# Kernel tuning notes

Hardware: AMD Instinct MI355X
Metric: run time of the kernel (lower is better)

## Reference

```python
import jax, jax.numpy as jnp
import numpy as np

B, S, D, H, E, K = 2, 2048, 1024, 4096, 8, 2


def setup_inputs() -> dict:
    key = jax.random.key(0)
    ks = jax.random.split(key, 5)
    x = jax.random.normal(ks[0], (B, S, D), dtype=jnp.float32)
    W = 0.02 * jax.random.normal(ks[1], (H, D), dtype=jnp.float32)
    bias = 0.02 * jax.random.normal(ks[2], (H,), dtype=jnp.float32)
    # alpha initialized near 1 (nn.Parameter(torch.ones(...)) + learned perturbation)
    alpha = 1.0 + 0.02 * jax.random.normal(ks[3], (E, D), dtype=jnp.float32)
    beta = 0.02 * jax.random.normal(ks[4], (E, D), dtype=jnp.float32)
    return {"x": x, "W": W, "bias": bias, "alpha": alpha, "beta": beta}


def reference(x, W, bias, alpha, beta):
    """MoEXLayer eval-mode forward (sparsity-aware routing + expert combine).

    x: [B,S,D], W: [H,D], bias: [H], alpha/beta: [E,D]. Returns [B,S,H].
    """
    E = alpha.shape[0]
    # --- Router: per-virtual-expert Gaussian pre-activation statistics ---
    # reconstructed_weight(alpha, beta) = W * alpha + beta  (column-wise affine)
    W_rec = W[None, :, :] * alpha[:, None, :] + beta[:, None, :]      # [E,H,D]
    mu_w = W_rec.mean(axis=1)                                          # [E,D]
    var_w = W_rec.var(axis=1)                                          # [E,D] (unbiased=False)
    mu_h = jnp.einsum('bsd,ed->bse', x, mu_w) + bias.mean()            # [B,S,E]
    sigma_h = jnp.sqrt(jnp.einsum('bsd,ed->bse', x * x, var_w) + 1e-8) # [B,S,E]
    router_logits = jax.lax.erf(mu_h / (jnp.sqrt(2.0) * sigma_h))      # [B,S,E]

    # --- Top-k routing: softmax over top-k logits, zeros elsewhere ---
    topk_vals, topk_idx = jax.lax.top_k(router_logits, K)              # [B,S,K]
    topk_w = jax.nn.softmax(topk_vals, axis=-1)                        # [B,S,K]
    router_weights = (jax.nn.one_hot(topk_idx, E, dtype=x.dtype)
                      * topk_w[..., None]).sum(axis=-2)                # [B,S,E]

    # --- Expert compute + combine (dispatch passes alpha only => beta=0) ---
    W_disp = W[None, :, :] * alpha[:, None, :]                         # [E,H,D]
    pre = jnp.einsum('bsd,ehd->bseh', x, W_disp) + bias                # [B,S,E,H]
    expert_out = jax.nn.relu(pre)
    out = jnp.einsum('bseh,bse->bsh', expert_out, router_weights)      # [B,S,H]
    return out
```

## Files before the change

### kernel.cpp

```cpp
#include <hip/hip_runtime.h>
#include <hip/hip_bf16.h>
#include <math.h>

#define DD 1024
#define HH 4096
#define EE 8
#define MTOK 4096
#define MROWS 8192

typedef __attribute__((ext_vector_type(8))) short bf16x8;
typedef __attribute__((ext_vector_type(4))) float f32x4;

__device__ __forceinline__ unsigned short f2bf(float x){
  __hip_bfloat16 h = __float2bfloat16(x);
  return *reinterpret_cast<unsigned short*>(&h);
}

__device__ __forceinline__ void gload16(const void* g, void* l){
  __builtin_amdgcn_global_load_lds((__attribute__((address_space(1))) void*)g,
                                   (__attribute__((address_space(3))) void*)l,
                                   16, 0, 0);
}

__global__ void cvt_w_kernel(const float4* __restrict__ W4, ushort4* __restrict__ Wb4){
  int i = blockIdx.x * 256 + threadIdx.x;
  float4 v = W4[i];
  ushort4 o;
  o.x = f2bf(v.x); o.y = f2bf(v.y); o.z = f2bf(v.z); o.w = f2bf(v.w);
  Wb4[i] = o;
}

__global__ void colstats_part_kernel(const float4* __restrict__ W4,
                                     float* __restrict__ pmean, float* __restrict__ pm2){
  int rc = blockIdx.x;
  int tid = threadIdx.x;
  double s0=0,s1=0,s2_=0,s3=0, q0=0,q1=0,q2=0,q3=0;
  for (int h = rc * 32; h < rc * 32 + 32; ++h){
    float4 w = W4[(size_t)h * 256 + tid];
    s0 += w.x; q0 += (double)w.x * w.x;
    s1 += w.y; q1 += (double)w.y * w.y;
    s2_ += w.z; q2 += (double)w.z * w.z;
    s3 += w.w; q3 += (double)w.w * w.w;
  }
  int d0 = rc * DD + tid * 4;
  pmean[d0]   = (float)s0;  pm2[d0]   = (float)q0;
  pmean[d0+1] = (float)s1;  pm2[d0+1] = (float)q1;
  pmean[d0+2] = (float)s2_; pm2[d0+2] = (float)q2;
  pmean[d0+3] = (float)s3;  pm2[d0+3] = (float)q3;
}

__global__ void colstats_final_kernel(const float* __restrict__ pmean,
                                      const float* __restrict__ pm2,
                                      double* __restrict__ cmean, double* __restrict__ cvar){
  int d = blockIdx.x * 256 + threadIdx.x;
  double s = 0.0, s2 = 0.0;
  for (int c = 0; c < 128; ++c){ s += (double)pmean[c * DD + d]; s2 += (double)pm2[c * DD + d]; }
  double m = s / (double)HH;
  cmean[d] = m;
  cvar[d]  = s2 / (double)HH - m * m;
}

__global__ void biasmean_kernel(const float* __restrict__ bias, double* __restrict__ bmean){
  __shared__ double red[256];
  double s = 0.0;
  for (int h = threadIdx.x; h < HH; h += 256) s += (double)bias[h];
  red[threadIdx.x] = s;
  __syncthreads();
  for (int k = 128; k > 0; k >>= 1){
    if (threadIdx.x < k) red[threadIdx.x] += red[threadIdx.x + k];
    __syncthreads();
  }
  if (threadIdx.x == 0) *bmean = red[0] / (double)HH;
}

__global__ void muvw_kernel(const float* __restrict__ alpha, const float* __restrict__ beta,
                            const double* __restrict__ cmean, const double* __restrict__ cvar,
                            float* __restrict__ muw, float* __restrict__ vw){
  int i = blockIdx.x * 256 + threadIdx.x;
  int d = i & (DD - 1);
  double a = (double)alpha[i];
  muw[i] = (float)(a * cmean[d] + (double)beta[i]);
  vw[i]  = (float)(a * a * cvar[d]);
}

__global__ __launch_bounds__(256) void router_kernel(const float4* __restrict__ x4,
                                                     const float4* __restrict__ alpha4,
                                                     const float4* __restrict__ muw4,
                                                     const float4* __restrict__ vw4,
                                                     const double* __restrict__ bmeanp,
                                                     unsigned short* __restrict__ Xs,
                                                     float2* __restrict__ wpair){
  int wv = threadIdx.x >> 6, lane = threadIdx.x & 63;
  int t = blockIdx.x * 4 + wv;
  const float4* xt = x4 + (size_t)t * 256;

  float4 xv[4];
  double mu[EE], s2[EE];
  #pragma unroll
  for (int e = 0; e < EE; ++e){ mu[e] = 0.0; s2[e] = 0.0; }

  #pragma unroll
  for (int r = 0; r < 4; ++r){
    int c = lane + 64 * r;
    float4 xf = xt[c];
    xv[r] = xf;
    float x2x = xf.x * xf.x, x2y = xf.y * xf.y, x2z = xf.z * xf.z, x2w = xf.w * xf.w;
    #pragma unroll
    for (int e = 0; e < EE; ++e){
      float4 m4 = muw4[e * 256 + c];
      float4 v4 = vw4[e * 256 + c];
      mu[e] += (double)xf.x * m4.x + (double)xf.y * m4.y
             + (double)xf.z * m4.z + (double)xf.w * m4.w;
      s2[e] += (double)x2x * v4.x + (double)x2y * v4.y
             + (double)x2z * v4.z + (double)x2w * v4.w;
    }
  }

  #pragma unroll
  for (int off = 32; off > 0; off >>= 1){
    #pragma unroll
    for (int e = 0; e < EE; ++e){
      mu[e] += __shfl_xor(mu[e], off);
      s2[e] += __shfl_xor(s2[e], off);
    }
  }

  double bm = *bmeanp;
  double z[EE];
  #pragma unroll
  for (int e = 0; e < EE; ++e){
    double m = mu[e] + bm;
    double v = s2[e] + 1e-8;
    z[e] = m / sqrt(2.0 * v);
  }
  int e1 = 0;
  #pragma unroll
  for (int e = 1; e < EE; ++e) if (z[e] > z[e1]) e1 = e;
  int e2 = -1;
  #pragma unroll
  for (int e = 0; e < EE; ++e){
    if (e == e1) continue;
    if (e2 < 0 || z[e] > z[e2]) e2 = e;
  }
  double lg1 = erf(z[e1]), lg2 = erf(z[e2]);
  double ex = exp(lg2 - lg1);
  float w1 = (float)(1.0 / (1.0 + ex));
  float w2 = (float)(ex / (1.0 + ex));
  if (lane == 0) wpair[t] = make_float2(w1, w2);

  const float4* a1 = alpha4 + (size_t)e1 * 256;
  const float4* a2 = alpha4 + (size_t)e2 * 256;
  ushort4* X1 = (ushort4*)(Xs + (size_t)(2 * t) * DD);
  ushort4* X2 = (ushort4*)(Xs + (size_t)(2 * t + 1) * DD);
  #pragma unroll
  for (int r = 0; r < 4; ++r){
    int c = lane + 64 * r;
    float4 xf = xv[r];
    float4 av = a1[c];
    X1[c] = make_ushort4(f2bf(xf.x * av.x), f2bf(xf.y * av.y),
                         f2bf(xf.z * av.z), f2bf(xf.w * av.w));
    av = a2[c];
    X2[c] = make_ushort4(f2bf(xf.x * av.x), f2bf(xf.y * av.y),
                         f2bf(xf.z * av.z), f2bf(xf.w * av.w));
  }
}

#define BM 128
#define BN 128
#define BK 32

__global__ __launch_bounds__(256) void gemm_kernel(const unsigned short* __restrict__ Xs,
                                                   const unsigned short* __restrict__ Wb,
                                                   const float* __restrict__ bias,
                                                   const float2* __restrict__ wpair,
                                                   float* __restrict__ out){
  __shared__ __align__(16) unsigned short As[BM * BK];
  __shared__ __align__(16) unsigned short Bs[BN * BK];

  int tid = threadIdx.x;
  int lane = tid & 63;
  int wv = tid >> 6;
  int wr = wv >> 1, wc = wv & 1;

  int bid = blockIdx.x;
  int swz = ((bid & 7) << 8) + (bid >> 3);
  int bm0 = (swz >> 5) * BM;
  int bn0 = (swz & 31) * BN;

  int arow = tid >> 2;
  int acol = (tid & 3) * 8;
  const unsigned short* Ag = Xs + (size_t)(bm0 + arow) * DD + acol;
  const unsigned short* Bg = Wb + (size_t)(bn0 + arow) * DD + acol;
  unsigned short* Asl = As + tid * 8;
  unsigned short* Bsl = Bs + tid * 8;

  f32x4 acc[4][4] = {};

  int l15 = lane & 15;
  int kb  = (lane >> 4) * 8;

  for (int kt = 0; kt < DD / BK; ++kt){
    int k0 = kt * BK;
    gload16(Ag + k0,            Asl);
    gload16(Ag + 64 * DD + k0,  Asl + 64 * BK);
    gload16(Bg + k0,            Bsl);
    gload16(Bg + 64 * DD + k0,  Bsl + 64 * BK);
    __syncthreads();

    bf16x8 af[4], bfr[4];
    #pragma unroll
    for (int mi = 0; mi < 4; ++mi)
      af[mi] = *(const bf16x8*)(As + (wr * 64 + mi * 16 + l15) * BK + kb);
    #pragma unroll
    for (int ni = 0; ni < 4; ++ni)
      bfr[ni] = *(const bf16x8*)(Bs + (wc * 64 + ni * 16 + l15) * BK + kb);

    #pragma unroll
    for (int mi = 0; mi < 4; ++mi)
      #pragma unroll
      for (int ni = 0; ni < 4; ++ni)
        acc[mi][ni] = __builtin_amdgcn_mfma_f32_16x16x32_bf16(af[mi], bfr[ni], acc[mi][ni], 0, 0, 0);

    __syncthreads();
  }

  #pragma unroll
  for (int mi = 0; mi < 4; ++mi){
    int rbase = wr * 64 + mi * 16 + ((lane >> 4) << 2);
    #pragma unroll
    for (int jp = 0; jp < 2; ++jp){
      int gm = bm0 + rbase + jp * 2;
      int t = gm >> 1;
      float2 w = wpair[t];
      #pragma unroll
      for (int ni = 0; ni < 4; ++ni){
        int gh = bn0 + wc * 64 + ni * 16 + l15;
        float bz = bias[gh];
        float v0 = acc[mi][ni][jp * 2]     + bz;
        float v1 = acc[mi][ni][jp * 2 + 1] + bz;
        out[(size_t)t * HH + gh] = w.x * fmaxf(v0, 0.f) + w.y * fmaxf(v1, 0.f);
      }
    }
  }
}

extern "C" void kernel_launch(void* const* d_in, const int* in_sizes, int n_in,
                              void* d_out, int out_size, void* d_ws, size_t ws_size,
                              hipStream_t stream) {
  const float* x     = (const float*)d_in[0];
  const float* W     = (const float*)d_in[1];
  const float* bias  = (const float*)d_in[2];
  const float* alpha = (const float*)d_in[3];
  const float* beta  = (const float*)d_in[4];
  float* out = (float*)d_out;

  char* ws = (char*)d_ws;
  unsigned short* Wb = (unsigned short*)ws;
  unsigned short* Xs = (unsigned short*)(ws + (8u << 20));
  float2* wpair      = (float2*)(ws + (24u << 20));
  double* cmean      = (double*)(ws + (24u << 20) + (64u << 10));
  double* cvar       = cmean + DD;
  double* bmean      = cvar + DD;
  float* pmean       = (float*)(ws + (24u << 20) + (128u << 10));
  float* pm2         = pmean + 128 * DD;
  float* muw         = (float*)(ws + (26u << 20));
  float* vw          = muw + EE * DD;

  cvt_w_kernel<<<4096, 256, 0, stream>>>((const float4*)W, (ushort4*)Wb);
  colstats_part_kernel<<<128, 256, 0, stream>>>((const float4*)W, pmean, pm2);
  colstats_final_kernel<<<4, 256, 0, stream>>>(pmean, pm2, cmean, cvar);
  biasmean_kernel<<<1, 256, 0, stream>>>(bias, bmean);
  muvw_kernel<<<32, 256, 0, stream>>>(alpha, beta, cmean, cvar, muw, vw);
  router_kernel<<<MTOK / 4, 256, 0, stream>>>((const float4*)x, (const float4*)alpha,
                                              (const float4*)muw, (const float4*)vw,
                                              bmean, Xs, wpair);
  gemm_kernel<<<(MROWS / BM) * (HH / BN), 256, 0, stream>>>(Xs, Wb, bias, wpair, out);
}
```

Measured before the change: 133.1 us.

## Double-buffer GEMM with BK=64, XOR-swizzled LDS, and fuse W conversion into stats

```diff
diff --git a/kernel.cpp b/kernel.cpp
--- a/kernel.cpp
+++ b/kernel.cpp
@@ -22,21 +22,14 @@
                                    16, 0, 0);
 }
 
-__global__ void cvt_w_kernel(const float4* __restrict__ W4, ushort4* __restrict__ Wb4){
-  int i = blockIdx.x * 256 + threadIdx.x;
-  float4 v = W4[i];
-  ushort4 o;
-  o.x = f2bf(v.x); o.y = f2bf(v.y); o.z = f2bf(v.z); o.w = f2bf(v.w);
-  Wb4[i] = o;
-}
-
-__global__ void colstats_part_kernel(const float4* __restrict__ W4,
-                                     float* __restrict__ pmean, float* __restrict__ pm2){
+__global__ void cvtstats_kernel(const float4* __restrict__ W4, ushort4* __restrict__ Wb4,
+                                float* __restrict__ pmean, float* __restrict__ pm2){
   int rc = blockIdx.x;
   int tid = threadIdx.x;
   double s0=0,s1=0,s2_=0,s3=0, q0=0,q1=0,q2=0,q3=0;
   for (int h = rc * 32; h < rc * 32 + 32; ++h){
     float4 w = W4[(size_t)h * 256 + tid];
+    Wb4[(size_t)h * 256 + tid] = make_ushort4(f2bf(w.x), f2bf(w.y), f2bf(w.z), f2bf(w.w));
     s0 += w.x; q0 += (double)w.x * w.x;
     s1 += w.y; q1 += (double)w.y * w.y;
     s2_ += w.z; q2 += (double)w.z * w.z;
@@ -167,61 +160,81 @@
 
 #define BM 128
 #define BN 128
-#define BK 32
-
-__global__ __launch_bounds__(256) void gemm_kernel(const unsigned short* __restrict__ Xs,
-                                                   const unsigned short* __restrict__ Wb,
-                                                   const float* __restrict__ bias,
-                                                   const float2* __restrict__ wpair,
-                                                   float* __restrict__ out){
-  __shared__ __align__(16) unsigned short As[BM * BK];
-  __shared__ __align__(16) unsigned short Bs[BN * BK];
-
-  int tid = threadIdx.x;
-  int lane = tid & 63;
-  int wv = tid >> 6;
+#define BKT 64
+#define NKT (DD / BKT)
+
+__global__ __launch_bounds__(256, 2) void gemm_kernel(const unsigned short* __restrict__ Xs,
+                                                      const unsigned short* __restrict__ Wb,
+                                                      const float* __restrict__ bias,
+                                                      const float2* __restrict__ wpair,
+                                                      float* __restrict__ out){
+  __shared__ __align__(16) unsigned short As[2 * 8192];
+  __shared__ __align__(16) unsigned short Bs[2 * 8192];
+
+  int tid = threadIdx.x, lane = tid & 63, wv = tid >> 6;
   int wr = wv >> 1, wc = wv & 1;
+  int l15 = lane & 15;
 
   int bid = blockIdx.x;
-  int swz = ((bid & 7) << 8) + (bid >> 3);
-  int bm0 = (swz >> 5) * BM;
-  int bn0 = (swz & 31) * BN;
-
-  int arow = tid >> 2;
-  int acol = (tid & 3) * 8;
-  const unsigned short* Ag = Xs + (size_t)(bm0 + arow) * DD + acol;
-  const unsigned short* Bg = Wb + (size_t)(bn0 + arow) * DD + acol;
-  unsigned short* Asl = As + tid * 8;
-  unsigned short* Bsl = Bs + tid * 8;
+  int ch = bid & 7, local = bid >> 3;
+  int mtile = ch * 8 + (local & 7);
+  int ntile = local >> 3;
+  int bm0 = mtile * BM, bn0 = ntile * BN;
+
+  int rl = lane >> 3;
+  int cg = (lane & 7) ^ rl;
+  const unsigned short* gA = Xs + (size_t)(bm0 + 32 * wv + rl) * DD + cg * 8;
+  const unsigned short* gB = Wb + (size_t)(bn0 + 32 * wv + rl) * DD + cg * 8;
+
+  int posr0 = (lane >> 4) ^ (l15 & 7);
+  int posr1 = (4 + (lane >> 4)) ^ (l15 & 7);
 
   f32x4 acc[4][4] = {};
 
-  int l15 = lane & 15;
-  int kb  = (lane >> 4) * 8;
-
-  for (int kt = 0; kt < DD / BK; ++kt){
-    int k0 = kt * BK;
-    gload16(Ag + k0,            Asl);
-    gload16(Ag + 64 * DD + k0,  Asl + 64 * BK);
-    gload16(Bg + k0,            Bsl);
-    gload16(Bg + 64 * DD + k0,  Bsl + 64 * BK);
-    __syncthreads();
-
-    bf16x8 af[4], bfr[4];
-    #pragma unroll
-    for (int mi = 0; mi < 4; ++mi)
-      af[mi] = *(const bf16x8*)(As + (wr * 64 + mi * 16 + l15) * BK + kb);
-    #pragma unroll
-    for (int ni = 0; ni < 4; ++ni)
-      bfr[ni] = *(const bf16x8*)(Bs + (wc * 64 + ni * 16 + l15) * BK + kb);
-
+  auto stage = [&](int kt, int slot){
+    int koff = kt * BKT;
+    #pragma unroll
+    for (int j = 0; j < 4; ++j){
+      gload16(gA + (size_t)(8 * j) * DD + koff, (void*)(As + slot * 8192 + (4 * wv + j) * 512));
+      gload16(gB + (size_t)(8 * j) * DD + koff, (void*)(Bs + slot * 8192 + (4 * wv + j) * 512));
+    }
+  };
+
+  stage(0, 0);
+  for (int t = 0; t < NKT; ++t){
+    if (t < NKT - 1){
+      stage(t + 1, (t + 1) & 1);
+      asm volatile("s_waitcnt vmcnt(8)" ::: "memory");
+    } else {
+      asm volatile("s_waitcnt vmcnt(0)" ::: "memory");
+    }
+    __builtin_amdgcn_s_barrier();
+
+    const unsigned short* Ab = As + (t & 1) * 8192;
+    const unsigned short* Bb = Bs + (t & 1) * 8192;
+    bf16x8 a0[4], a1[4], b0[4], b1[4];
+    #pragma unroll
+    for (int i = 0; i < 4; ++i){
+      int ra = (wr * 64 + i * 16 + l15) * 64;
+      a0[i] = *(const bf16x8*)(Ab + ra + posr0 * 8);
+      a1[i] = *(const bf16x8*)(Ab + ra + posr1 * 8);
+      int rb = (wc * 64 + i * 16 + l15) * 64;
+      b0[i] = *(const bf16x8*)(Bb + rb + posr0 * 8);
+      b1[i] = *(const bf16x8*)(Bb + rb + posr1 * 8);
+    }
+
+    __builtin_amdgcn_s_setprio(1);
     #pragma unroll
     for (int mi = 0; mi < 4; ++mi)
       #pragma unroll
-      for (int ni = 0; ni < 4; ++ni)
-        acc[mi][ni] = __builtin_amdgcn_mfma_f32_16x16x32_bf16(af[mi], bfr[ni], acc[mi][ni], 0, 0, 0);
-
-    __syncthreads();
+      for (int ni = 0; ni < 4; ++ni){
+        acc[mi][ni] = __builtin_amdgcn_mfma_f32_16x16x32_bf16(a0[mi], b0[ni], acc[mi][ni], 0, 0, 0);
+        acc[mi][ni] = __builtin_amdgcn_mfma_f32_16x16x32_bf16(a1[mi], b1[ni], acc[mi][ni], 0, 0, 0);
+      }
+    __builtin_amdgcn_s_setprio(0);
+
+    asm volatile("s_waitcnt lgkmcnt(0)" ::: "memory");
+    __builtin_amdgcn_s_barrier();
   }
 
   #pragma unroll
@@ -266,8 +279,7 @@
   float* muw         = (float*)(ws + (26u << 20));
   float* vw          = muw + EE * DD;
 
-  cvt_w_kernel<<<4096, 256, 0, stream>>>((const float4*)W, (ushort4*)Wb);
-  colstats_part_kernel<<<128, 256, 0, stream>>>((const float4*)W, pmean, pm2);
+  cvtstats_kernel<<<128, 256, 0, stream>>>((const float4*)W, (ushort4*)Wb, pmean, pm2);
   colstats_final_kernel<<<4, 256, 0, stream>>>(pmean, pm2, cmean, cvar);
   biasmean_kernel<<<1, 256, 0, stream>>>(bias, bmean);
   muvw_kernel<<<32, 256, 0, stream>>>(alpha, beta, cmean, cvar, muw, vw);
```

Result: faster. 124.9 us (-6.2%).
